# Performance work log

Hardware: AMD Instinct MI355X
Metric: run time of the kernel (lower is better)

The kernel has to match this reference:

```python
import jax, jax.numpy as jnp
import numpy as np
from jax import lax

B, T, I, H, L, O = 256, 512, 64, 256, 2, 1


def _lstm_dir(x, w_ih, w_hh, b_ih, b_hh, reverse):
    # x: [B,T,Din]; w_ih: [4H,Din]; w_hh: [4H,H]; biases: [4H]
    Bn = x.shape[0]
    Hn = w_hh.shape[1]
    # precompute input projection for all timesteps
    xp = jnp.einsum('btd,gd->btg', x, w_ih) + b_ih + b_hh  # [B,T,4H]
    xp = jnp.swapaxes(xp, 0, 1)  # [T,B,4H]
    h0 = jnp.zeros((Bn, Hn), x.dtype)
    c0 = jnp.zeros((Bn, Hn), x.dtype)

    def step(carry, g_t):
        h, c = carry
        gates = g_t + h @ w_hh.T  # [B,4H]
        i, f, g, o = jnp.split(gates, 4, axis=-1)  # PyTorch gate order
        c = jax.nn.sigmoid(f) * c + jax.nn.sigmoid(i) * jnp.tanh(g)
        h = jax.nn.sigmoid(o) * jnp.tanh(c)
        return (h, c), h

    _, hs = lax.scan(step, (h0, c0), xp, reverse=reverse)  # hs: [T,B,H], time-aligned
    return jnp.swapaxes(hs, 0, 1)  # [B,T,H]


def setup_inputs() -> dict:
    key = jax.random.key(0)
    ks = jax.random.split(key, 20)
    s = 1.0 / np.sqrt(H)
    u = lambda k, shp: jax.random.uniform(k, shp, jnp.float32, -s, s)
    d = {
        'x': jax.random.normal(ks[0], (B, T, I), jnp.float32),
        # layer 0, forward and reverse directions
        'w_ih_l0': u(ks[1], (4 * H, I)), 'w_hh_l0': u(ks[2], (4 * H, H)),
        'b_ih_l0': u(ks[3], (4 * H,)), 'b_hh_l0': u(ks[4], (4 * H,)),
        'w_ih_l0r': u(ks[5], (4 * H, I)), 'w_hh_l0r': u(ks[6], (4 * H, H)),
        'b_ih_l0r': u(ks[7], (4 * H,)), 'b_hh_l0r': u(ks[8], (4 * H,)),
        # layer 1 (input dim = 2H from bidirectional concat)
        'w_ih_l1': u(ks[9], (4 * H, 2 * H)), 'w_hh_l1': u(ks[10], (4 * H, H)),
        'b_ih_l1': u(ks[11], (4 * H,)), 'b_hh_l1': u(ks[12], (4 * H,)),
        'w_ih_l1r': u(ks[13], (4 * H, 2 * H)), 'w_hh_l1r': u(ks[14], (4 * H, H)),
        'b_ih_l1r': u(ks[15], (4 * H,)), 'b_hh_l1r': u(ks[16], (4 * H,)),
        # fc head
        'fc_w': u(ks[17], (O, 2 * H)), 'fc_b': u(ks[18], (O,)),
    }
    return d


def reference(x, w_ih_l0, w_hh_l0, b_ih_l0, b_hh_l0,
              w_ih_l0r, w_hh_l0r, b_ih_l0r, b_hh_l0r,
              w_ih_l1, w_hh_l1, b_ih_l1, b_hh_l1,
              w_ih_l1r, w_hh_l1r, b_ih_l1r, b_hh_l1r,
              fc_w, fc_b):
    # layer 0
    h_fwd = _lstm_dir(x, w_ih_l0, w_hh_l0, b_ih_l0, b_hh_l0, reverse=False)
    h_bwd = _lstm_dir(x, w_ih_l0r, w_hh_l0r, b_ih_l0r, b_hh_l0r, reverse=True)
    h = jnp.concatenate([h_fwd, h_bwd], axis=-1)  # [B,T,2H]
    # layer 1
    h_fwd = _lstm_dir(h, w_ih_l1, w_hh_l1, b_ih_l1, b_hh_l1, reverse=False)
    h_bwd = _lstm_dir(h, w_ih_l1r, w_hh_l1r, b_ih_l1r, b_hh_l1r, reverse=True)
    h = jnp.concatenate([h_fwd, h_bwd], axis=-1)  # [B,T,2H]
    # fc on last timestep
    return h[:, -1, :] @ fc_w.T + fc_b  # [B,O]
```

## Files before the change

### kernel.cpp

```cpp
#include <hip/hip_runtime.h>

typedef __bf16 bf16_t;
typedef bf16_t bf16x8 __attribute__((ext_vector_type(8)));
typedef bf16_t bf16x4 __attribute__((ext_vector_type(4)));
typedef float f32x4 __attribute__((ext_vector_type(4)));

#define B_SZ 256
#define T_SZ 512
#define H_SZ 256
#define SCOPE_AGENT __HIP_MEMORY_SCOPE_AGENT
#define SENT32 0x7FC17FC1u

__device__ __forceinline__ float sigm(float x) { return 1.f / (1.f + __expf(-x)); }
__device__ __forceinline__ float tanhx(float x) {
  x = fminf(fmaxf(x, -15.f), 15.f);
  float e = __expf(-2.f * x);
  return (1.f - e) / (1.f + e);
}
__device__ __forceinline__ uint32_t pack_bf16x2(float a, float b) {
  union { bf16_t h[2]; uint32_t u; } v;
  v.h[0] = (bf16_t)a; v.h[1] = (bf16_t)b; return v.u;
}
__device__ __forceinline__ void st32_agent(uint32_t* p, uint32_t v) {
  __hip_atomic_store(p, v, __ATOMIC_RELAXED, SCOPE_AGENT);
}
__device__ __forceinline__ uint64_t ld64_agent(const uint64_t* p) {
  return __hip_atomic_load(p, __ATOMIC_RELAXED, SCOPE_AGENT);
}
__device__ __forceinline__ bool okv(uint64_t v) {
  return ((uint32_t)v != SENT32) & ((uint32_t)(v >> 32) != SENT32);
}
#define MFMA(a, b, c) __builtin_amdgcn_mfma_f32_16x16x32_bf16((a), (b), (c), 0, 0, 0)

__global__ __launch_bounds__(256, 1) void l0_scan(
    const bf16_t* __restrict__ xbf,
    const bf16_t* __restrict__ wih_f, const bf16_t* __restrict__ whhhi_f,
    const bf16_t* __restrict__ whhlo_f, const float* __restrict__ bias_f,
    const bf16_t* __restrict__ wih_b, const bf16_t* __restrict__ whhhi_b,
    const bf16_t* __restrict__ whhlo_b, const float* __restrict__ bias_b,
    bf16_t* __restrict__ h0) {
  const int id = blockIdx.x;
  const int dir = id >> 7, bt = (id >> 3) & 15, ct = id & 7;
  const bf16_t* __restrict__ wih  = dir ? wih_b : wih_f;
  const bf16_t* __restrict__ whhh = dir ? whhhi_b : whhhi_f;
  const bf16_t* __restrict__ whhl = dir ? whhlo_b : whhlo_f;
  const float*  __restrict__ bias = dir ? bias_b : bias_f;

  const int tid = threadIdx.x;
  const int lane = tid & 63, wv = tid >> 6, l15 = lane & 15, quad = lane >> 4;
  const int b0 = bt * 16;

  __shared__ bf16_t hbl[16][264];
  __shared__ float  gl[16][132];

  bf16x8 wfi[2][2], wfh[2][8], wfl[2][8];
#pragma unroll
  for (int p = 0; p < 2; ++p) {
    const int gc = (wv * 2 + p) * 16 + l15;
    const int row = (gc >> 5) * H_SZ + ct * 32 + (gc & 31);
#pragma unroll
    for (int kt = 0; kt < 2; ++kt)
      wfi[p][kt] = *(const bf16x8*)(wih + (size_t)row * 64 + kt * 32 + quad * 8);
#pragma unroll
    for (int kt = 0; kt < 8; ++kt) {
      wfh[p][kt] = *(const bf16x8*)(whhh + (size_t)row * H_SZ + kt * 32 + quad * 8);
      wfl[p][kt] = *(const bf16x8*)(whhl + (size_t)row * H_SZ + kt * 32 + quad * 8);
    }
  }
  const int erow = tid >> 4, ecol = 2 * (tid & 15);
  const int gj = ct * 32 + ecol;
  float bia[4][2];
#pragma unroll
  for (int g = 0; g < 4; ++g) {
    bia[g][0] = bias[g * H_SZ + gj];
    bia[g][1] = bias[g * H_SZ + gj + 1];
  }
  float2 c2 = {0.f, 0.f};
  const bf16_t* xrow = xbf + (size_t)(b0 + l15) * T_SZ * 64;
  const int prow = tid >> 4, pcq = (tid & 15) * 4;

  for (int s = 0; s < T_SZ; ++s) {
    const int t = dir ? (T_SZ - 1 - s) : s;
    f32x4 acc0 = {0.f, 0.f, 0.f, 0.f}, acc1 = {0.f, 0.f, 0.f, 0.f};
#pragma unroll
    for (int kt = 0; kt < 2; ++kt) {
      bf16x8 xa = *(const bf16x8*)(xrow + t * 64 + kt * 32 + quad * 8);
      acc0 = MFMA(xa, wfi[0][kt], acc0);
      acc1 = MFMA(xa, wfi[1][kt], acc1);
    }
    if (s == 0) {
      for (int i = tid; i < 16 * 264 / 2; i += 256) ((uint32_t*)hbl)[i] = 0u;
    } else {
      const int tp = dir ? (t + 1) : (t - 1);
      const uint64_t* src =
          (const uint64_t*)(h0 + ((size_t)tp * B_SZ + b0 + prow) * 512 + dir * H_SZ) + pcq;
      uint64_t v0, v1, v2, v3;
      for (;;) {
        v0 = ld64_agent(src);     v1 = ld64_agent(src + 1);
        v2 = ld64_agent(src + 2); v3 = ld64_agent(src + 3);
        if (okv(v0) && okv(v1) && okv(v2) && okv(v3)) break;
      }
      uint64_t* dst = (uint64_t*)&hbl[prow][pcq * 4];
      dst[0] = v0; dst[1] = v1; dst[2] = v2; dst[3] = v3;
    }
    __syncthreads();
#pragma unroll
    for (int kt = 0; kt < 8; ++kt) {
      bf16x8 ha = *(const bf16x8*)&hbl[l15][kt * 32 + quad * 8];
      acc0 = MFMA(ha, wfh[0][kt], acc0);
      acc0 = MFMA(ha, wfl[0][kt], acc0);
      acc1 = MFMA(ha, wfh[1][kt], acc1);
      acc1 = MFMA(ha, wfl[1][kt], acc1);
    }
#pragma unroll
    for (int r = 0; r < 4; ++r) {
      gl[quad * 4 + r][(wv * 2 + 0) * 16 + l15] = acc0[r];
      gl[quad * 4 + r][(wv * 2 + 1) * 16 + l15] = acc1[r];
    }
    __syncthreads();
    {
      float hv[2];
#pragma unroll
      for (int u = 0; u < 2; ++u) {
        float iv = sigm(gl[erow][0 * 32 + ecol + u] + bia[0][u]);
        float fv = sigm(gl[erow][1 * 32 + ecol + u] + bia[1][u]);
        float gv = tanhx(gl[erow][2 * 32 + ecol + u] + bia[2][u]);
        float ov = sigm(gl[erow][3 * 32 + ecol + u] + bia[3][u]);
        float cp = u ? c2.y : c2.x;
        float cn = fv * cp + iv * gv;
        if (u) c2.y = cn; else c2.x = cn;
        hv[u] = ov * tanhx(cn);
      }
      st32_agent((uint32_t*)(h0 + ((size_t)t * B_SZ + b0 + erow) * 512 + dir * H_SZ + gj),
                 pack_bf16x2(hv[0], hv[1]));
    }
  }
}

__global__ __launch_bounds__(512, 2) void l1_scan(
    const bf16_t* __restrict__ h0,
    const bf16_t* __restrict__ wih, const bf16_t* __restrict__ whhh,
    const bf16_t* __restrict__ whhl, const float* __restrict__ bias,
    bf16_t* __restrict__ h1f, bf16_t* __restrict__ hg1) {
  const int bt = blockIdx.x >> 3, ct = blockIdx.x & 7;
  bf16_t* hgs = hg1 + (size_t)bt * T_SZ * 4096;

  const int tid = threadIdx.x;
  const int lane = tid & 63, wv = tid >> 6, l15 = lane & 15, quad = lane >> 4;
  const int b0 = bt * 16;

  __shared__ bf16_t ibl[2][16][520];
  __shared__ bf16_t hbl[16][264];
  __shared__ float  gl[16][132];

  const int gc = wv * 16 + l15;
  const int row = (gc >> 5) * H_SZ + ct * 32 + (gc & 31);
  bf16x8 wfi[16], wfh[8], wfl[8];
#pragma unroll
  for (int kt = 0; kt < 16; ++kt)
    wfi[kt] = *(const bf16x8*)(wih + (size_t)row * 512 + kt * 32 + quad * 8);
#pragma unroll
  for (int kt = 0; kt < 8; ++kt) {
    wfh[kt] = *(const bf16x8*)(whhh + (size_t)row * H_SZ + kt * 32 + quad * 8);
    wfl[kt] = *(const bf16x8*)(whhl + (size_t)row * H_SZ + kt * 32 + quad * 8);
  }
  const int et = tid & 255;
  const int erow = et >> 4, ecol = 2 * (et & 15);
  const int gj = ct * 32 + ecol;
  float bia[4][2];
#pragma unroll
  for (int g = 0; g < 4; ++g) {
    bia[g][0] = bias[g * H_SZ + gj];
    bia[g][1] = bias[g * H_SZ + gj + 1];
  }
  float2 c2 = {0.f, 0.f};
  const int prow = tid >> 5, pcq = (tid & 31) * 2;

  {
    const int r = tid >> 5, cc = (tid & 31) * 16;
    const bf16_t* src = h0 + ((size_t)(b0 + r)) * 512 + cc;
    *(bf16x8*)&ibl[0][r][cc]     = *(const bf16x8*)(src);
    *(bf16x8*)&ibl[0][r][cc + 8] = *(const bf16x8*)(src + 8);
  }
  __syncthreads();

  for (int s = 0; s < T_SZ; ++s) {
    const int cur = s & 1, nxt = cur ^ 1;
    if (s + 1 < T_SZ) {
      const int r = tid >> 5, cc = (tid & 31) * 16;
      const bf16_t* src = h0 + ((size_t)(s + 1) * B_SZ + b0 + r) * 512 + cc;
      *(bf16x8*)&ibl[nxt][r][cc]     = *(const bf16x8*)(src);
      *(bf16x8*)&ibl[nxt][r][cc + 8] = *(const bf16x8*)(src + 8);
    }
    f32x4 acc = {0.f, 0.f, 0.f, 0.f};
#pragma unroll
    for (int kt = 0; kt < 16; ++kt) {
      bf16x8 a = *(const bf16x8*)&ibl[cur][l15][kt * 32 + quad * 8];
      acc = MFMA(a, wfi[kt], acc);
    }
    if (s == 0) {
      for (int i = tid; i < 16 * 264 / 2; i += 512) ((uint32_t*)hbl)[i] = 0u;
    } else {
      const uint64_t* src =
          (const uint64_t*)(hgs + (size_t)(s - 1) * 4096 + prow * H_SZ) + pcq;
      uint64_t v0, v1;
      for (;;) {
        v0 = ld64_agent(src); v1 = ld64_agent(src + 1);
        if (okv(v0) && okv(v1)) break;
      }
      uint64_t* dst = (uint64_t*)&hbl[prow][pcq * 4];
      dst[0] = v0; dst[1] = v1;
    }
    __syncthreads();
#pragma unroll
    for (int kt = 0; kt < 8; ++kt) {
      bf16x8 ha = *(const bf16x8*)&hbl[l15][kt * 32 + quad * 8];
      acc = MFMA(ha, wfh[kt], acc);
      acc = MFMA(ha, wfl[kt], acc);
    }
#pragma unroll
    for (int r = 0; r < 4; ++r) gl[quad * 4 + r][wv * 16 + l15] = acc[r];
    __syncthreads();
    if (tid < 256) {
      float hv[2];
#pragma unroll
      for (int u = 0; u < 2; ++u) {
        float iv = sigm(gl[erow][0 * 32 + ecol + u] + bia[0][u]);
        float fv = sigm(gl[erow][1 * 32 + ecol + u] + bia[1][u]);
        float gv = tanhx(gl[erow][2 * 32 + ecol + u] + bia[2][u]);
        float ov = sigm(gl[erow][3 * 32 + ecol + u] + bia[3][u]);
        float cp = u ? c2.y : c2.x;
        float cn = fv * cp + iv * gv;
        if (u) c2.y = cn; else c2.x = cn;
        hv[u] = ov * tanhx(cn);
      }
      uint32_t pk = pack_bf16x2(hv[0], hv[1]);
      st32_agent((uint32_t*)(hgs + (size_t)s * 4096 + erow * H_SZ + gj), pk);
      if (s == T_SZ - 1)
        *(uint32_t*)(h1f + (size_t)(b0 + erow) * H_SZ + gj) = pk;
    }
  }
}

__global__ __launch_bounds__(256) void l1b_step(
    const bf16_t* __restrict__ h0, const bf16_t* __restrict__ wih_r,
    const float* __restrict__ bias_r, bf16_t* __restrict__ h1b) {
  const int bt = blockIdx.x >> 2, ct = blockIdx.x & 3;
  const int tid = threadIdx.x, lane = tid & 63, wv = tid >> 6;
  const int l15 = lane & 15, quad = lane >> 4;
  const int c0 = ct * 64 + wv * 16;
  const bf16_t* arow = h0 + ((size_t)(T_SZ - 1) * B_SZ + bt * 16 + l15) * 512;
  f32x4 acc[4] = {{0,0,0,0},{0,0,0,0},{0,0,0,0},{0,0,0,0}};
#pragma unroll 4
  for (int kt = 0; kt < 16; ++kt) {
    bf16x8 a = *(const bf16x8*)(arow + kt * 32 + quad * 8);
#pragma unroll
    for (int g = 0; g < 4; ++g) {
      bf16x8 w = *(const bf16x8*)(wih_r + (size_t)(g * H_SZ + c0 + l15) * 512 + kt * 32 + quad * 8);
      acc[g] = MFMA(a, w, acc[g]);
    }
  }
  const int j = c0 + l15;
  const float bi = bias_r[j], bg = bias_r[2 * H_SZ + j], bo = bias_r[3 * H_SZ + j];
#pragma unroll
  for (int r = 0; r < 4; ++r) {
    const int row = bt * 16 + quad * 4 + r;
    float iv = sigm(acc[0][r] + bi);
    float gv = tanhx(acc[2][r] + bg);
    float ov = sigm(acc[3][r] + bo);
    float cn = iv * gv;
    h1b[(size_t)row * H_SZ + j] = (bf16_t)(ov * tanhx(cn));
  }
}

__global__ void k_cvt4(const float* __restrict__ s, bf16_t* __restrict__ d, int n4) {
  int i = blockIdx.x * 256 + threadIdx.x;
  if (i < n4) {
    float4 v = ((const float4*)s)[i];
    bf16x4 o; o[0] = (bf16_t)v.x; o[1] = (bf16_t)v.y; o[2] = (bf16_t)v.z; o[3] = (bf16_t)v.w;
    ((bf16x4*)d)[i] = o;
  }
}
__global__ void k_split(const float* __restrict__ s, bf16_t* __restrict__ hi,
                        bf16_t* __restrict__ lo, int n) {
  int i = blockIdx.x * 256 + threadIdx.x;
  if (i < n) {
    float v = s[i];
    bf16_t h = (bf16_t)v;
    hi[i] = h;
    lo[i] = (bf16_t)(v - (float)h);
  }
}
__global__ void k_bias(const float* __restrict__ a, const float* __restrict__ b,
                       float* __restrict__ d, int n) {
  int i = blockIdx.x * 256 + threadIdx.x;
  if (i < n) d[i] = a[i] + b[i];
}
__global__ void k_fill4(uint4* __restrict__ p, int n) {
  int i = blockIdx.x * 256 + threadIdx.x;
  if (i < n) p[i] = make_uint4(SENT32, SENT32, SENT32, SENT32);
}
__global__ void k_fc(const bf16_t* __restrict__ hf, const bf16_t* __restrict__ hb,
                     const float* __restrict__ fw, const float* __restrict__ fb,
                     float* __restrict__ out) {
  int b = threadIdx.x;
  float s = fb[0];
  const bf16_t* pf = hf + (size_t)b * H_SZ;
  const bf16_t* pb = hb + (size_t)b * H_SZ;
  for (int j = 0; j < H_SZ; ++j) s += fw[j] * (float)pf[j];
  for (int j = 0; j < H_SZ; ++j) s += fw[H_SZ + j] * (float)pb[j];
  out[b] = s;
}

extern "C" void kernel_launch(void* const* d_in, const int* in_sizes, int n_in,
                              void* d_out, int out_size, void* d_ws, size_t ws_size,
                              hipStream_t stream) {
  (void)in_sizes; (void)n_in; (void)out_size; (void)ws_size;
  const float* x      = (const float*)d_in[0];
  const float* wih[4] = {(const float*)d_in[1], (const float*)d_in[5],
                         (const float*)d_in[9], (const float*)d_in[13]};
  const float* whh[4] = {(const float*)d_in[2], (const float*)d_in[6],
                         (const float*)d_in[10], (const float*)d_in[14]};
  const float* bih[4] = {(const float*)d_in[3], (const float*)d_in[7],
                         (const float*)d_in[11], (const float*)d_in[15]};
  const float* bhh[4] = {(const float*)d_in[4], (const float*)d_in[8],
                         (const float*)d_in[12], (const float*)d_in[16]};
  const float* fcw = (const float*)d_in[17];
  const float* fcb = (const float*)d_in[18];
  float* out = (float*)d_out;

  char* p = (char*)d_ws;
  auto take = [&](size_t bytes) { char* r = p; p += (bytes + 255) & ~(size_t)255; return r; };
  const int KinL[4] = {64, 64, 512, 512};
  bf16_t* wihb[4]; float* biasc[4]; bf16_t* whhhi[3]; bf16_t* whhlo[3];
  for (int k = 0; k < 4; ++k) {
    wihb[k]  = (bf16_t*)take((size_t)1024 * KinL[k] * 2);
    biasc[k] = (float*)take(1024 * 4);
  }
  for (int k = 0; k < 3; ++k) {
    whhhi[k] = (bf16_t*)take((size_t)1024 * 256 * 2);
    whhlo[k] = (bf16_t*)take((size_t)1024 * 256 * 2);
  }
  bf16_t* xbf = (bf16_t*)take((size_t)B_SZ * T_SZ * 64 * 2);
  bf16_t* h1f = (bf16_t*)take((size_t)B_SZ * H_SZ * 2);
  bf16_t* h1b = (bf16_t*)take((size_t)B_SZ * H_SZ * 2);
  char* sbeg = p;
  bf16_t* h0  = (bf16_t*)take((size_t)T_SZ * B_SZ * 512 * 2);
  bf16_t* hg1 = (bf16_t*)take((size_t)16 * T_SZ * 4096 * 2);
  size_t sbytes = (size_t)(p - sbeg);

  k_cvt4<<<dim3(8192), 256, 0, stream>>>(x, xbf, (B_SZ * T_SZ * 64) / 4);
  for (int k = 0; k < 4; ++k) {
    k_cvt4<<<dim3((1024 * KinL[k] / 4 + 255) / 256), 256, 0, stream>>>(
        wih[k], wihb[k], 1024 * KinL[k] / 4);
    k_bias<<<dim3(4), 256, 0, stream>>>(bih[k], bhh[k], biasc[k], 1024);
  }
  for (int k = 0; k < 3; ++k)
    k_split<<<dim3(1024), 256, 0, stream>>>(whh[k], whhhi[k], whhlo[k], 1024 * 256);
  {
    int n4 = (int)(sbytes / 16);
    k_fill4<<<dim3((n4 + 255) / 256), 256, 0, stream>>>((uint4*)sbeg, n4);
  }

  l0_scan<<<dim3(256), 256, 0, stream>>>(
      xbf, wihb[0], whhhi[0], whhlo[0], biasc[0],
           wihb[1], whhhi[1], whhlo[1], biasc[1], h0);
  l1_scan<<<dim3(128), 512, 0, stream>>>(
      h0, wihb[2], whhhi[2], whhlo[2], biasc[2], h1f, hg1);
  l1b_step<<<dim3(64), 256, 0, stream>>>(h0, wihb[3], biasc[3], h1b);

  k_fc<<<dim3(1), 256, 0, stream>>>(h1f, h1b, fcw, fcb, out);
}
```

Baseline: 2.276 ms.

## Widen l0_scan to 512 threads and remap block indices across column tiles

The layer-0 recurrent kernel now runs 8 waves per block, each owning one 16-column gate tile instead of two. This halves the MFMA chain length per wave and spreads the polling loads across more threads. Block-index mapping for both scan kernels is reordered so that blocks sharing a batch tile differ in the high bits, changing their placement on CUs/XCDs. The l1 prefetch now loads into registers before the spin-wait and writes to LDS afterwards, so the global load latency overlaps the wait. In exchange, the extra waves add register pressure and more synchronisation participants per block.

New measurement: 2.082 ms. 1.09x faster.

```diff
diff --git a/kernel.cpp b/kernel.cpp
--- a/kernel.cpp
+++ b/kernel.cpp
@@ -32,7 +32,7 @@
 }
 #define MFMA(a, b, c) __builtin_amdgcn_mfma_f32_16x16x32_bf16((a), (b), (c), 0, 0, 0)
 
-__global__ __launch_bounds__(256, 1) void l0_scan(
+__global__ __launch_bounds__(512, 2) void l0_scan(
     const bf16_t* __restrict__ xbf,
     const bf16_t* __restrict__ wih_f, const bf16_t* __restrict__ whhhi_f,
     const bf16_t* __restrict__ whhlo_f, const float* __restrict__ bias_f,
@@ -40,7 +40,9 @@
     const bf16_t* __restrict__ whhlo_b, const float* __restrict__ bias_b,
     bf16_t* __restrict__ h0) {
   const int id = blockIdx.x;
-  const int dir = id >> 7, bt = (id >> 3) & 15, ct = id & 7;
+  const int ct = id >> 5;
+  const int g  = id & 31;
+  const int dir = g >> 4, bt = g & 15;
   const bf16_t* __restrict__ wih  = dir ? wih_b : wih_f;
   const bf16_t* __restrict__ whhh = dir ? whhhi_b : whhhi_f;
   const bf16_t* __restrict__ whhl = dir ? whhlo_b : whhlo_f;
@@ -53,72 +55,63 @@
   __shared__ bf16_t hbl[16][264];
   __shared__ float  gl[16][132];
 
-  bf16x8 wfi[2][2], wfh[2][8], wfl[2][8];
-#pragma unroll
-  for (int p = 0; p < 2; ++p) {
-    const int gc = (wv * 2 + p) * 16 + l15;
-    const int row = (gc >> 5) * H_SZ + ct * 32 + (gc & 31);
-#pragma unroll
-    for (int kt = 0; kt < 2; ++kt)
-      wfi[p][kt] = *(const bf16x8*)(wih + (size_t)row * 64 + kt * 32 + quad * 8);
-#pragma unroll
-    for (int kt = 0; kt < 8; ++kt) {
-      wfh[p][kt] = *(const bf16x8*)(whhh + (size_t)row * H_SZ + kt * 32 + quad * 8);
-      wfl[p][kt] = *(const bf16x8*)(whhl + (size_t)row * H_SZ + kt * 32 + quad * 8);
-    }
-  }
-  const int erow = tid >> 4, ecol = 2 * (tid & 15);
+  const int gc = wv * 16 + l15;
+  const int row = (gc >> 5) * H_SZ + ct * 32 + (gc & 31);
+  bf16x8 wfi[2], wfh[8], wfl[8];
+#pragma unroll
+  for (int kt = 0; kt < 2; ++kt)
+    wfi[kt] = *(const bf16x8*)(wih + (size_t)row * 64 + kt * 32 + quad * 8);
+#pragma unroll
+  for (int kt = 0; kt < 8; ++kt) {
+    wfh[kt] = *(const bf16x8*)(whhh + (size_t)row * H_SZ + kt * 32 + quad * 8);
+    wfl[kt] = *(const bf16x8*)(whhl + (size_t)row * H_SZ + kt * 32 + quad * 8);
+  }
+  const int et = tid & 255;
+  const int erow = et >> 4, ecol = 2 * (et & 15);
   const int gj = ct * 32 + ecol;
   float bia[4][2];
 #pragma unroll
-  for (int g = 0; g < 4; ++g) {
-    bia[g][0] = bias[g * H_SZ + gj];
-    bia[g][1] = bias[g * H_SZ + gj + 1];
+  for (int gg = 0; gg < 4; ++gg) {
+    bia[gg][0] = bias[gg * H_SZ + gj];
+    bia[gg][1] = bias[gg * H_SZ + gj + 1];
   }
   float2 c2 = {0.f, 0.f};
   const bf16_t* xrow = xbf + (size_t)(b0 + l15) * T_SZ * 64;
-  const int prow = tid >> 4, pcq = (tid & 15) * 4;
+  const int prow = tid >> 5, pcq = (tid & 31) * 2;
 
   for (int s = 0; s < T_SZ; ++s) {
     const int t = dir ? (T_SZ - 1 - s) : s;
-    f32x4 acc0 = {0.f, 0.f, 0.f, 0.f}, acc1 = {0.f, 0.f, 0.f, 0.f};
+    f32x4 acc = {0.f, 0.f, 0.f, 0.f};
 #pragma unroll
     for (int kt = 0; kt < 2; ++kt) {
       bf16x8 xa = *(const bf16x8*)(xrow + t * 64 + kt * 32 + quad * 8);
-      acc0 = MFMA(xa, wfi[0][kt], acc0);
-      acc1 = MFMA(xa, wfi[1][kt], acc1);
+      acc = MFMA(xa, wfi[kt], acc);
     }
     if (s == 0) {
-      for (int i = tid; i < 16 * 264 / 2; i += 256) ((uint32_t*)hbl)[i] = 0u;
+      for (int i = tid; i < 16 * 264 / 2; i += 512) ((uint32_t*)hbl)[i] = 0u;
     } else {
       const int tp = dir ? (t + 1) : (t - 1);
       const uint64_t* src =
           (const uint64_t*)(h0 + ((size_t)tp * B_SZ + b0 + prow) * 512 + dir * H_SZ) + pcq;
-      uint64_t v0, v1, v2, v3;
+      uint64_t v0, v1;
       for (;;) {
-        v0 = ld64_agent(src);     v1 = ld64_agent(src + 1);
-        v2 = ld64_agent(src + 2); v3 = ld64_agent(src + 3);
-        if (okv(v0) && okv(v1) && okv(v2) && okv(v3)) break;
+        v0 = ld64_agent(src); v1 = ld64_agent(src + 1);
+        if (okv(v0) && okv(v1)) break;
       }
       uint64_t* dst = (uint64_t*)&hbl[prow][pcq * 4];
-      dst[0] = v0; dst[1] = v1; dst[2] = v2; dst[3] = v3;
+      dst[0] = v0; dst[1] = v1;
     }
     __syncthreads();
 #pragma unroll
     for (int kt = 0; kt < 8; ++kt) {
       bf16x8 ha = *(const bf16x8*)&hbl[l15][kt * 32 + quad * 8];
-      acc0 = MFMA(ha, wfh[0][kt], acc0);
-      acc0 = MFMA(ha, wfl[0][kt], acc0);
-      acc1 = MFMA(ha, wfh[1][kt], acc1);
-      acc1 = MFMA(ha, wfl[1][kt], acc1);
-    }
-#pragma unroll
-    for (int r = 0; r < 4; ++r) {
-      gl[quad * 4 + r][(wv * 2 + 0) * 16 + l15] = acc0[r];
-      gl[quad * 4 + r][(wv * 2 + 1) * 16 + l15] = acc1[r];
-    }
+      acc = MFMA(ha, wfh[kt], acc);
+      acc = MFMA(ha, wfl[kt], acc);
+    }
+#pragma unroll
+    for (int r = 0; r < 4; ++r) gl[quad * 4 + r][wv * 16 + l15] = acc[r];
     __syncthreads();
-    {
+    if (tid < 256) {
       float hv[2];
 #pragma unroll
       for (int u = 0; u < 2; ++u) {
@@ -142,7 +135,8 @@
     const bf16_t* __restrict__ wih, const bf16_t* __restrict__ whhh,
     const bf16_t* __restrict__ whhl, const float* __restrict__ bias,
     bf16_t* __restrict__ h1f, bf16_t* __restrict__ hg1) {
-  const int bt = blockIdx.x >> 3, ct = blockIdx.x & 7;
+  const int id = blockIdx.x;
+  const int ct = id >> 4, bt = id & 15;
   bf16_t* hgs = hg1 + (size_t)bt * T_SZ * 4096;
 
   const int tid = threadIdx.x;
@@ -175,22 +169,22 @@
   }
   float2 c2 = {0.f, 0.f};
   const int prow = tid >> 5, pcq = (tid & 31) * 2;
+  const int fr = tid >> 5, fcc = (tid & 31) * 16;
 
   {
-    const int r = tid >> 5, cc = (tid & 31) * 16;
-    const bf16_t* src = h0 + ((size_t)(b0 + r)) * 512 + cc;
-    *(bf16x8*)&ibl[0][r][cc]     = *(const bf16x8*)(src);
-    *(bf16x8*)&ibl[0][r][cc + 8] = *(const bf16x8*)(src + 8);
+    const bf16_t* src = h0 + ((size_t)(b0 + fr)) * 512 + fcc;
+    *(bf16x8*)&ibl[0][fr][fcc]     = *(const bf16x8*)(src);
+    *(bf16x8*)&ibl[0][fr][fcc + 8] = *(const bf16x8*)(src + 8);
   }
   __syncthreads();
 
   for (int s = 0; s < T_SZ; ++s) {
     const int cur = s & 1, nxt = cur ^ 1;
+    bf16x8 pf0, pf1;
     if (s + 1 < T_SZ) {
-      const int r = tid >> 5, cc = (tid & 31) * 16;
-      const bf16_t* src = h0 + ((size_t)(s + 1) * B_SZ + b0 + r) * 512 + cc;
-      *(bf16x8*)&ibl[nxt][r][cc]     = *(const bf16x8*)(src);
-      *(bf16x8*)&ibl[nxt][r][cc + 8] = *(const bf16x8*)(src + 8);
+      const bf16_t* src = h0 + ((size_t)(s + 1) * B_SZ + b0 + fr) * 512 + fcc;
+      pf0 = *(const bf16x8*)(src);
+      pf1 = *(const bf16x8*)(src + 8);
     }
     f32x4 acc = {0.f, 0.f, 0.f, 0.f};
 #pragma unroll
@@ -210,6 +204,10 @@
       }
       uint64_t* dst = (uint64_t*)&hbl[prow][pcq * 4];
       dst[0] = v0; dst[1] = v1;
+    }
+    if (s + 1 < T_SZ) {
+      *(bf16x8*)&ibl[nxt][fr][fcc]     = pf0;
+      *(bf16x8*)&ibl[nxt][fr][fcc + 8] = pf1;
     }
     __syncthreads();
 #pragma unroll
@@ -362,7 +360,7 @@
     k_fill4<<<dim3((n4 + 255) / 256), 256, 0, stream>>>((uint4*)sbeg, n4);
   }
 
-  l0_scan<<<dim3(256), 256, 0, stream>>>(
+  l0_scan<<<dim3(256), 512, 0, stream>>>(
       xbf, wihb[0], whhhi[0], whhlo[0], biasc[0],
            wihb[1], whhhi[1], whhlo[1], biasc[1], h0);
   l1_scan<<<dim3(128), 512, 0, stream>>>(
```
